# Performance work log

Measured on AMD Instinct MI355X. Metric: run time of the kernel, lower is better.

The kernel has to match this reference:

```python
import jax, jax.numpy as jnp
import numpy as np

B, L, D, DEPTH, FF, VOCAB = 2, 2048, 1024, 4, 4096, 32000

def setup_inputs():
    key = jax.random.key(0)
    ks = jax.random.split(key, 16)
    n = lambda k, s, sc: jax.random.normal(k, s, dtype=jnp.float32) * sc
    sw = 0.01 / float(np.sqrt(D))  # xavier_normal with gain 0.01 on square dims
    return dict(
        tokens=jax.random.randint(ks[0], (B, L), 0, VOCAB),
        emb=n(ks[1], (VOCAB, D), 0.02),
        Wz=n(ks[2], (DEPTH, D, D), sw), bz=jnp.zeros((DEPTH, D)),
        Wza=n(ks[3], (DEPTH, D, D), sw), bza=jnp.zeros((DEPTH, D)),
        Wy=n(ks[4], (DEPTH, D, D), sw), by=jnp.zeros((DEPTH, D)),
        Wya=n(ks[5], (DEPTH, D, D), sw), bya=jnp.zeros((DEPTH, D)),
        lc_re=n(ks[6], (DEPTH, D), 1.0), lc_im=n(ks[7], (DEPTH, D), 1.0),
        g_in=jnp.ones((DEPTH, D)), g_sc=jnp.ones((DEPTH, D)), g_ffn=jnp.ones((DEPTH, D)),
        Wf=n(ks[8], (DEPTH, D, FF), 0.02), bf=jnp.zeros((DEPTH, FF)),
        Wfa=n(ks[9], (DEPTH, D, FF), 0.02), bfa=jnp.zeros((DEPTH, FF)),
        Wfo=n(ks[10], (DEPTH, FF, D), 0.02), bfo=jnp.zeros((DEPTH, D)),
        ln_w=jnp.ones((D,)), ln_b=jnp.zeros((D,)),
        Wout=n(ks[11], (D, VOCAB), 0.02), bout=jnp.zeros((VOCAB,)),
    )

def _silu(x):
    return x * jax.nn.sigmoid(x)

def _rms(x, w, eps=1e-6):
    return x * jax.lax.rsqrt(jnp.mean(x * x, axis=-1, keepdims=True) + eps) * w

def reference(tokens, emb, Wz, bz, Wza, bza, Wy, by, Wya, bya, lc_re, lc_im,
              g_in, g_sc, g_ffn, Wf, bf, Wfa, bfa, Wfo, bfo, ln_w, ln_b, Wout, bout):
    Bq, Lq = tokens.shape
    # Embedding with max_norm=1: torch renorms accessed rows to norm <= 1
    e = emb[tokens]
    nrm = jnp.linalg.norm(e, axis=-1, keepdims=True)
    x = e * jnp.minimum(1.0, 1.0 / jnp.maximum(nrm, 1e-7))
    # Decaying phazor kernel (shared across layers; phazor_angle_scale is a fixed buffer)
    angle = jnp.power(0.001, jnp.linspace(0.0, 1.0, D))
    ln_ph = (1e-5 + 1j * angle).astype(jnp.complex64)      # [D]
    t = jnp.arange(Lq, dtype=jnp.float32)
    ph = jnp.exp(t[:, None] * ln_ph[None, :])              # [L, D] complex
    pf = jnp.fft.fft(ph, n=2 * Lq, axis=0)                 # [2L, D]
    decay = jnp.exp(ln_ph)                                 # [D]
    for i in range(DEPTH):
        # --- SConv sublayer (pre-RMSNorm + residual) ---
        xr = x
        xn = _rms(x, g_sc[i])
        z = (xn @ Wz[i] + bz[i]) * _silu(xn @ Wza[i] + bza[i])
        zf = jnp.fft.fft(z.astype(jnp.complex64), n=2 * Lq, axis=1)
        h = jnp.fft.ifft(zf * pf[None], axis=1)[:, :Lq]    # inner-chunk causal decaying conv
        lc = (lc_re[i] + 1j * lc_im[i]).astype(jnp.complex64)
        h = h + lc[None, None, :] * ph[None] * decay[None, None, :]  # cross-chunk state carry
        y = (_rms(h.real, g_in[i]) @ Wy[i] + by[i]) * _silu(xn @ Wya[i] + bya[i])
        x = xr + y
        # --- FFN SwiGLU sublayer (pre-RMSNorm + residual) ---
        xr = x
        xn = _rms(x, g_ffn[i])
        x = xr + ((xn @ Wf[i] + bf[i]) * _silu(xn @ Wfa[i] + bfa[i])) @ Wfo[i] + bfo[i]
    # Final LayerNorm + vocab projection
    mu = jnp.mean(x, axis=-1, keepdims=True)
    var = jnp.mean((x - mu) ** 2, axis=-1, keepdims=True)
    x = (x - mu) * jax.lax.rsqrt(var + 1e-5) * ln_w + ln_b
    return x @ Wout + bout
```

## Files before the change

### kernel.cpp

```cpp
#include <hip/hip_runtime.h>
#include <math.h>

typedef __attribute__((ext_vector_type(8))) short bf16x8;
typedef __attribute__((ext_vector_type(4))) float f32x4;

#define DEVI __device__ __forceinline__

DEVI short f2bf(float f) {
  unsigned u = __builtin_bit_cast(unsigned, f);
  return (short)((u + 0x7fffu + ((u >> 16) & 1u)) >> 16);
}

DEVI float silu_f(float v) { return v / (1.0f + expf(-v)); }

DEVI void async16(const void* g, void* l) {
  __builtin_amdgcn_global_load_lds(
      (const __attribute__((address_space(1))) void*)g,
      (__attribute__((address_space(3))) void*)l, 16, 0, 0);
}

template <int N>
DEVI void waitvm() { asm volatile("s_waitcnt vmcnt(%0)" ::"i"(N) : "memory"); }
DEVI void barrier_mem() { asm volatile("s_barrier" ::: "memory"); }

template <int NROWT>
DEVI void tile_map(int* bx, int* by) {
  const int nwg = gridDim.x;
  const int lin = blockIdx.x;
  const int q = nwg >> 3;
  const int wgid = (lin & 7) * q + (lin >> 3);
  *by = wgid % NROWT;
  *bx = wgid / NROWT;
}


template <int MODE, int BM, int BN, int NBUF, bool NT>
__global__ __launch_bounds__(256) void gemm_k(const short* __restrict__ A,
                                              const short* __restrict__ BT,
                                              const float* __restrict__ bias,
                                              void* __restrict__ outp,
                                              int N, int K) {
  constexpr int MF = BM / 32, NF = BN / 32;
  constexpr int PBB = (BM + BN) * 64;
  constexpr int DEPTH = NBUF - 1;
  constexpr int L = (BM + BN) / 64;
  __shared__ __align__(16) char lds[NBUF * PBB];
  int bx, by;
  tile_map<4096 / BM>(&bx, &by);
  const int row0 = by * BM, col0 = bx * BN;
  const int t = threadIdx.x, w = t >> 6, lane = t & 63;
  const int wr = w >> 1, wc = w & 1;
  f32x4 acc[MF][NF] = {};

  const int srow = t >> 2;
  const int sslot = (t & 3) ^ ((t >> 3) & 3);
  const char* gA0 = (const char*)A + ((size_t)(row0 + srow) * K) * 2 + sslot * 16;
  const char* gB0 = (const char*)BT + ((size_t)(col0 + srow) * K) * 2 + sslot * 16;
  const size_t ccstep = (size_t)K * 128;
  const int wb = w << 10;
  const int lr = lane & 15, ks = lane >> 4;

  const int NIT = K >> 5;
  auto stage = [&](int buf, int it) {
    char* dst = lds + buf * PBB;
    const size_t io = (size_t)it * 64;
#pragma unroll
    for (int cc = 0; cc < BM / 64; ++cc)
      async16(gA0 + io + cc * ccstep, dst + cc * 4096 + wb);
#pragma unroll
    for (int cc = 0; cc < BN / 64; ++cc)
      async16(gB0 + io + cc * ccstep, dst + BM * 64 + cc * 4096 + wb);
  };

#pragma unroll
  for (int pit = 0; pit < DEPTH; ++pit) stage(pit, pit);

  for (int it = 0; it < NIT; ++it) {
    const int rem = NIT - it;
    if (rem >= DEPTH) waitvm<L * (DEPTH - 1)>();
    else if (rem == 2) waitvm<L>();
    else waitvm<0>();
    barrier_mem();
    if (it + DEPTH < NIT) stage((it + DEPTH) % NBUF, it + DEPTH);
    const char* base = lds + (it % NBUF) * PBB;
    bf16x8 af[MF], bfr[NF];
#pragma unroll
    for (int m = 0; m < MF; ++m) {
      const int r = wr * (BM / 2) + m * 16 + lr;
      af[m] = *(const bf16x8*)(base + r * 64 + ((ks ^ ((r >> 1) & 3)) << 4));
    }
#pragma unroll
    for (int n = 0; n < NF; ++n) {
      const int r = wc * (BN / 2) + n * 16 + lr;
      bfr[n] = *(const bf16x8*)(base + BM * 64 + r * 64 + ((ks ^ ((r >> 1) & 3)) << 4));
    }
#pragma unroll
    for (int m = 0; m < MF; ++m)
#pragma unroll
      for (int n = 0; n < NF; ++n)
        acc[m][n] = __builtin_amdgcn_mfma_f32_16x16x32_bf16(af[m], bfr[n], acc[m][n], 0, 0, 0);
    __builtin_amdgcn_sched_barrier(0);
  }

  const int orow = row0 + wr * (BM / 2) + (ks << 2);
  const int ocol = col0 + wc * (BN / 2) + lr;
#pragma unroll
  for (int m = 0; m < MF; ++m) {
#pragma unroll
    for (int n = 0; n < NF; ++n) {
      const int c = ocol + (n << 4);
      const float bv = bias[c];
#pragma unroll
      for (int i = 0; i < 4; ++i) {
        const int r = orow + (m << 4) + i;
        const size_t idx = (size_t)r * N + c;
        float v = acc[m][n][i] + bv;
        if (MODE == 0) {
          if (NT) __builtin_nontemporal_store(v, &((float*)outp)[idx]);
          else ((float*)outp)[idx] = v;
        } else {
          ((float*)outp)[idx] += v;
        }
      }
    }
  }
}

template <int MODE, int BM, int NBUF>
__global__ __launch_bounds__(256) void gemm2_k(const short* __restrict__ A1,
                                               const short* __restrict__ A2,
                                               const short* __restrict__ BT1,
                                               const short* __restrict__ BT2,
                                               const float* __restrict__ bias1,
                                               const float* __restrict__ bias2,
                                               void* __restrict__ outp,
                                               int N, int K) {
  constexpr bool DUALA = (MODE == 1);
  constexpr int MF = BM / 32;
  constexpr int ABYTES = BM * 64 * (DUALA ? 2 : 1);
  constexpr int PBB = ABYTES + 16384;
  constexpr int DEPTH = NBUF - 1;
  constexpr int L = (DUALA ? 2 * (BM / 64) : (BM / 64)) + 4;
  __shared__ __align__(16) char lds[NBUF * PBB];
  int bx, by;
  tile_map<4096 / BM>(&bx, &by);
  const int row0 = by * BM, col0 = bx << 7;
  const int t = threadIdx.x, w = t >> 6, lane = t & 63;
  const int wr = w >> 1, wc = w & 1;
  f32x4 acc1[MF][4] = {}, acc2[MF][4] = {};

  const int srow = t >> 2;
  const int sslot = (t & 3) ^ ((t >> 3) & 3);
  const size_t arow = ((size_t)(row0 + srow) * K) * 2 + sslot * 16;
  const size_t brow = ((size_t)(col0 + srow) * K) * 2 + sslot * 16;
  const char* gA1 = (const char*)A1 + arow;
  const char* gA2 = (const char*)A2 + arow;
  const char* gB1 = (const char*)BT1 + brow;
  const char* gB2 = (const char*)BT2 + brow;
  const size_t ccstep = (size_t)K * 128;
  const int wb = w << 10;
  const int lr = lane & 15, ks = lane >> 4;

  const int NIT = K >> 5;
  auto stage = [&](int buf, int it) {
    char* dst = lds + buf * PBB;
    const size_t io = (size_t)it * 64;
#pragma unroll
    for (int cc = 0; cc < BM / 64; ++cc) {
      async16(gA1 + io + cc * ccstep, dst + cc * 4096 + wb);
      if constexpr (DUALA)
        async16(gA2 + io + cc * ccstep, dst + BM * 64 + cc * 4096 + wb);
    }
    async16(gB1 + io, dst + ABYTES + wb);
    async16(gB1 + io + ccstep, dst + ABYTES + 4096 + wb);
    async16(gB2 + io, dst + ABYTES + 8192 + wb);
    async16(gB2 + io + ccstep, dst + ABYTES + 8192 + 4096 + wb);
  };

#pragma unroll
  for (int pit = 0; pit < DEPTH; ++pit) stage(pit, pit);

  for (int it = 0; it < NIT; ++it) {
    const int rem = NIT - it;
    if (rem >= DEPTH) waitvm<L * (DEPTH - 1)>();
    else if (rem == 2) waitvm<L>();
    else waitvm<0>();
    barrier_mem();
    if (it + DEPTH < NIT) stage((it + DEPTH) % NBUF, it + DEPTH);
    const char* base = lds + (it % NBUF) * PBB;
    bf16x8 af1[MF], af2[MF], bf1[4], bf2[4];
#pragma unroll
    for (int m = 0; m < MF; ++m) {
      const int r = wr * (BM / 2) + m * 16 + lr;
      const int off = r * 64 + ((ks ^ ((r >> 1) & 3)) << 4);
      af1[m] = *(const bf16x8*)(base + off);
      if constexpr (DUALA) af2[m] = *(const bf16x8*)(base + BM * 64 + off);
    }
#pragma unroll
    for (int n = 0; n < 4; ++n) {
      const int r = wc * 64 + n * 16 + lr;
      const int off = r * 64 + ((ks ^ ((r >> 1) & 3)) << 4);
      bf1[n] = *(const bf16x8*)(base + ABYTES + off);
      bf2[n] = *(const bf16x8*)(base + ABYTES + 8192 + off);
    }
#pragma unroll
    for (int m = 0; m < MF; ++m)
#pragma unroll
      for (int n = 0; n < 4; ++n) {
        acc1[m][n] = __builtin_amdgcn_mfma_f32_16x16x32_bf16(af1[m], bf1[n], acc1[m][n], 0, 0, 0);
        acc2[m][n] = __builtin_amdgcn_mfma_f32_16x16x32_bf16(DUALA ? af2[m] : af1[m], bf2[n],
                                                             acc2[m][n], 0, 0, 0);
      }
    __builtin_amdgcn_sched_barrier(0);
  }

  const int orow = row0 + wr * (BM / 2) + (ks << 2);
  const int ocol = col0 + (wc << 6) + lr;
#pragma unroll
  for (int m = 0; m < MF; ++m) {
#pragma unroll
    for (int n = 0; n < 4; ++n) {
      const int c = ocol + (n << 4);
      const float bv1 = bias1[c], bv2 = bias2[c];
#pragma unroll
      for (int i = 0; i < 4; ++i) {
        const int r = orow + (m << 4) + i;
        const size_t idx = (size_t)r * N + c;
        const float g = (acc1[m][n][i] + bv1) * silu_f(acc2[m][n][i] + bv2);
        if (MODE == 0) ((float*)outp)[idx] = g;
        else if (MODE == 1) ((float*)outp)[idx] += g;
        else ((short*)outp)[idx] = f2bf(g);
      }
    }
  }
}

__global__ __launch_bounds__(256) void transp_k(const float* __restrict__ W,
                                                short* __restrict__ WT,
                                                int R, int C) {
  __shared__ float tile[32][33];
  const size_t moff = (size_t)blockIdx.z * R * C;
  const float* Wp = W + moff;
  short* Tp = WT + moff;
  const int c0 = blockIdx.x << 5, r0 = blockIdx.y << 5;
  const int tx = threadIdx.x, ty = threadIdx.y;
#pragma unroll
  for (int i = 0; i < 4; ++i)
    tile[ty + 8 * i][tx] = Wp[(size_t)(r0 + ty + 8 * i) * C + (c0 + tx)];
  __syncthreads();
#pragma unroll
  for (int i = 0; i < 4; ++i)
    Tp[(size_t)(c0 + ty + 8 * i) * R + (r0 + tx)] = f2bf(tile[tx][ty + 8 * i]);
}

__global__ __launch_bounds__(256) void embed_k(const int* __restrict__ tok,
                                               const float* __restrict__ emb,
                                               float* __restrict__ x) {
  const int row = blockIdx.x, t = threadIdx.x, w = t >> 6, lane = t & 63;
  const int token = tok[row];
  float4 v = ((const float4*)(emb + (size_t)token * 1024))[t];
  float ss = v.x * v.x + v.y * v.y + v.z * v.z + v.w * v.w;
#pragma unroll
  for (int off = 32; off; off >>= 1) ss += __shfl_xor(ss, off, 64);
  __shared__ float red[4];
  if (lane == 0) red[w] = ss;
  __syncthreads();
  const float nrm = sqrtf(red[0] + red[1] + red[2] + red[3]);
  const float sc = fminf(1.0f, 1.0f / fmaxf(nrm, 1e-7f));
  v.x *= sc; v.y *= sc; v.z *= sc; v.w *= sc;
  ((float4*)(x + (size_t)row * 1024))[t] = v;
}

__global__ __launch_bounds__(256) void rms_k(const float* __restrict__ x,
                                             const float* __restrict__ g,
                                             short* __restrict__ o) {
  const int row = blockIdx.x, t = threadIdx.x, w = t >> 6, lane = t & 63;
  float4 v = ((const float4*)(x + (size_t)row * 1024))[t];
  float ss = v.x * v.x + v.y * v.y + v.z * v.z + v.w * v.w;
#pragma unroll
  for (int off = 32; off; off >>= 1) ss += __shfl_xor(ss, off, 64);
  __shared__ float red[4];
  if (lane == 0) red[w] = ss;
  __syncthreads();
  const float sc = rsqrtf((red[0] + red[1] + red[2] + red[3]) * (1.0f / 1024.0f) + 1e-6f);
  float4 gv = ((const float4*)g)[t];
  short4 ov = make_short4(f2bf(v.x * sc * gv.x), f2bf(v.y * sc * gv.y),
                          f2bf(v.z * sc * gv.z), f2bf(v.w * sc * gv.w));
  *(short4*)(o + (size_t)row * 1024 + 4 * t) = ov;
}

__global__ __launch_bounds__(256) void ln_k(const float* __restrict__ x,
                                            const float* __restrict__ lw,
                                            const float* __restrict__ lb,
                                            short* __restrict__ o) {
  const int row = blockIdx.x, t = threadIdx.x, w = t >> 6, lane = t & 63;
  float4 v = ((const float4*)(x + (size_t)row * 1024))[t];
  float s1 = v.x + v.y + v.z + v.w;
  float s2 = v.x * v.x + v.y * v.y + v.z * v.z + v.w * v.w;
#pragma unroll
  for (int off = 32; off; off >>= 1) {
    s1 += __shfl_xor(s1, off, 64);
    s2 += __shfl_xor(s2, off, 64);
  }
  __shared__ float red[8];
  if (lane == 0) { red[w] = s1; red[4 + w] = s2; }
  __syncthreads();
  const float mu = (red[0] + red[1] + red[2] + red[3]) * (1.0f / 1024.0f);
  const float ex2 = (red[4] + red[5] + red[6] + red[7]) * (1.0f / 1024.0f);
  const float rs = rsqrtf(ex2 - mu * mu + 1e-5f);
  float4 wv = ((const float4*)lw)[t];
  float4 bv = ((const float4*)lb)[t];
  short4 ov = make_short4(f2bf((v.x - mu) * rs * wv.x + bv.x),
                          f2bf((v.y - mu) * rs * wv.y + bv.y),
                          f2bf((v.z - mu) * rs * wv.z + bv.z),
                          f2bf((v.w - mu) * rs * wv.w + bv.w));
  *(short4*)(o + (size_t)row * 1024 + 4 * t) = ov;
}

DEVI void decay_of(int d, float* dr, float* di) {
  const float ang = powf(1e-3f, (float)d * (1.0f / 1023.0f));
  float sn, cs;
  sincosf(ang, &sn, &cs);
  const float mag = expf(1e-5f);
  *dr = mag * cs; *di = mag * sn;
}

__global__ __launch_bounds__(256) void s1_k(const float* __restrict__ z,
                                            float* __restrict__ Er, float* __restrict__ Ei) {
  const int d = (blockIdx.x << 8) + threadIdx.x;
  const int c = blockIdx.y, b = blockIdx.z;
  float dr, di;
  decay_of(d, &dr, &di);
  const float* zp = z + ((size_t)(b * 2048 + c * 64) << 10) + d;
  float sr = 0.0f, si = 0.0f;
  for (int k = 0; k < 64; ++k) {
    float zv = zp[(size_t)k << 10];
    float nr = dr * sr - di * si + zv;
    si = dr * si + di * sr;
    sr = nr;
  }
  const int idx = ((b << 5) + c) * 1024 + d;
  Er[idx] = sr; Ei[idx] = si;
}

__global__ __launch_bounds__(256) void s2_k(const float* __restrict__ Er,
                                            const float* __restrict__ Ei,
                                            float* __restrict__ Sr, float* __restrict__ Si) {
  const int gid = (blockIdx.x << 8) + threadIdx.x;
  const int b = gid >> 10, d = gid & 1023;
  float dr, di;
  decay_of(d, &dr, &di);
  float ar = dr, ai = di;
#pragma unroll
  for (int q = 0; q < 6; ++q) { float nr = ar * ar - ai * ai; ai = 2.0f * ar * ai; ar = nr; }
  float sr = 0.0f, si = 0.0f;
  for (int c = 0; c < 32; ++c) {
    const int idx = ((b << 5) + c) * 1024 + d;
    Sr[idx] = sr; Si[idx] = si;
    const float er = Er[idx], ei = Ei[idx];
    const float nr = ar * sr - ai * si + er;
    si = ar * si + ai * sr + ei;
    sr = nr;
  }
}

__global__ __launch_bounds__(256) void s3_k(const float* __restrict__ z,
                                            const float* __restrict__ Sr,
                                            const float* __restrict__ Si,
                                            const float* __restrict__ lcre,
                                            const float* __restrict__ lcim,
                                            float* __restrict__ h) {
  const int d = (blockIdx.x << 8) + threadIdx.x;
  const int c = blockIdx.y, b = blockIdx.z;
  float dr, di;
  decay_of(d, &dr, &di);
  float ar = dr, ai = di;
#pragma unroll
  for (int q = 0; q < 6; ++q) { float nr = ar * ar - ai * ai; ai = 2.0f * ar * ai; ar = nr; }
  float wr = 1.0f, wi = 0.0f, br = ar, bi = ai;
  int e = c;
  while (e) {
    if (e & 1) { float nr = wr * br - wi * bi; wi = wr * bi + wi * br; wr = nr; }
    float nb = br * br - bi * bi; bi = 2.0f * br * bi; br = nb;
    e >>= 1;
  }
  { float nr = wr * dr - wi * di; wi = wr * di + wi * dr; wr = nr; }
  const int idx = ((b << 5) + c) * 1024 + d;
  float sr = Sr[idx], si = Si[idx];
  const float lr_ = lcre[d], li_ = lcim[d];
  const size_t base = ((size_t)(b * 2048 + c * 64) << 10) + d;
  for (int k = 0; k < 64; ++k) {
    const float zv = z[base + ((size_t)k << 10)];
    const float nr = dr * sr - di * si + zv;
    si = dr * si + di * sr;
    sr = nr;
    h[base + ((size_t)k << 10)] = sr + lr_ * wr - li_ * wi;
    const float nw = wr * dr - wi * di;
    wi = wr * di + wi * dr;
    wr = nw;
  }
}

extern "C" void kernel_launch(void* const* d_in, const int* in_sizes, int n_in,
                              void* d_out, int out_size, void* d_ws, size_t ws_size,
                              hipStream_t stream) {
  const int* tokens = (const int*)d_in[0];
  const float* emb = (const float*)d_in[1];
  const float* Wz = (const float*)d_in[2];
  const float* bz = (const float*)d_in[3];
  const float* Wza = (const float*)d_in[4];
  const float* bza = (const float*)d_in[5];
  const float* Wy = (const float*)d_in[6];
  const float* by = (const float*)d_in[7];
  const float* Wya = (const float*)d_in[8];
  const float* bya = (const float*)d_in[9];
  const float* lc_re = (const float*)d_in[10];
  const float* lc_im = (const float*)d_in[11];
  const float* g_in = (const float*)d_in[12];
  const float* g_sc = (const float*)d_in[13];
  const float* g_ffn = (const float*)d_in[14];
  const float* Wf = (const float*)d_in[15];
  const float* bf = (const float*)d_in[16];
  const float* Wfa = (const float*)d_in[17];
  const float* bfa = (const float*)d_in[18];
  const float* Wfo = (const float*)d_in[19];
  const float* bfo = (const float*)d_in[20];
  const float* ln_w = (const float*)d_in[21];
  const float* ln_b = (const float*)d_in[22];
  const float* Wout = (const float*)d_in[23];
  const float* bout = (const float*)d_in[24];

  char* p = (char*)d_ws;
  float* xb = (float*)p;   p += (size_t)4096 * 1024 * 4;
  float* zb = (float*)p;   p += (size_t)4096 * 1024 * 4;
  float* hb = (float*)p;   p += (size_t)4096 * 1024 * 4;
  float* Er = (float*)p;   p += (size_t)2 * 32 * 1024 * 4;
  float* Ei = (float*)p;   p += (size_t)2 * 32 * 1024 * 4;
  float* Sr = (float*)p;   p += (size_t)2 * 32 * 1024 * 4;
  float* Si = (float*)p;   p += (size_t)2 * 32 * 1024 * 4;
  short* xnb = (short*)p;  p += (size_t)4096 * 1024 * 2;
  short* hnb = (short*)p;  p += (size_t)4096 * 1024 * 2;
  short* gb = (short*)p;   p += (size_t)4096 * 4096 * 2;
  short* WzT = (short*)p;  p += (size_t)4 * 1024 * 1024 * 2;
  short* WzaT = (short*)p; p += (size_t)4 * 1024 * 1024 * 2;
  short* WyT = (short*)p;  p += (size_t)4 * 1024 * 1024 * 2;
  short* WyaT = (short*)p; p += (size_t)4 * 1024 * 1024 * 2;
  short* WfT = (short*)p;  p += (size_t)4 * 1024 * 4096 * 2;
  short* WfaT = (short*)p; p += (size_t)4 * 1024 * 4096 * 2;
  short* WfoT = (short*)p; p += (size_t)4 * 1024 * 4096 * 2;
  short* WoutT = (short*)p; p += (size_t)32000 * 1024 * 2;

  const dim3 tb(32, 8);
  transp_k<<<dim3(32, 32, 4), tb, 0, stream>>>(Wz, WzT, 1024, 1024);
  transp_k<<<dim3(32, 32, 4), tb, 0, stream>>>(Wza, WzaT, 1024, 1024);
  transp_k<<<dim3(32, 32, 4), tb, 0, stream>>>(Wy, WyT, 1024, 1024);
  transp_k<<<dim3(32, 32, 4), tb, 0, stream>>>(Wya, WyaT, 1024, 1024);
  transp_k<<<dim3(128, 32, 4), tb, 0, stream>>>(Wf, WfT, 1024, 4096);
  transp_k<<<dim3(128, 32, 4), tb, 0, stream>>>(Wfa, WfaT, 1024, 4096);
  transp_k<<<dim3(32, 128, 4), tb, 0, stream>>>(Wfo, WfoT, 4096, 1024);
  transp_k<<<dim3(1000, 32, 1), tb, 0, stream>>>(Wout, WoutT, 1024, 32000);

  embed_k<<<4096, 256, 0, stream>>>(tokens, emb, xb);

  for (int i = 0; i < 4; ++i) {
    const size_t dd = (size_t)i * 1024 * 1024;
    const size_t dv = (size_t)i * 1024;
    const size_t dw = (size_t)i * 1024 * 4096;
    const size_t df = (size_t)i * 4096;
    rms_k<<<4096, 256, 0, stream>>>(xb, g_sc + dv, xnb);
    gemm2_k<0, 64, 3><<<512, 256, 0, stream>>>(xnb, xnb, WzT + dd, WzaT + dd, bz + dv, bza + dv,
                                               zb, 1024, 1024);
    s1_k<<<dim3(4, 32, 2), 256, 0, stream>>>(zb, Er, Ei);
    s2_k<<<8, 256, 0, stream>>>(Er, Ei, Sr, Si);
    s3_k<<<dim3(4, 32, 2), 256, 0, stream>>>(zb, Sr, Si, lc_re + dv, lc_im + dv, hb);
    rms_k<<<4096, 256, 0, stream>>>(hb, g_in + dv, hnb);
    gemm2_k<1, 64, 2><<<512, 256, 0, stream>>>(hnb, xnb, WyT + dd, WyaT + dd, by + dv, bya + dv,
                                               xb, 1024, 1024);
    rms_k<<<4096, 256, 0, stream>>>(xb, g_ffn + dv, xnb);
    gemm2_k<2, 64, 3><<<2048, 256, 0, stream>>>(xnb, xnb, WfT + dw, WfaT + dw, bf + df, bfa + df,
                                                gb, 4096, 1024);
    gemm_k<4, 64, 128, 4, false><<<512, 256, 0, stream>>>(gb, WfoT + dw, bfo + dv, xb, 1024, 4096);
  }

  ln_k<<<4096, 256, 0, stream>>>(xb, ln_w, ln_b, xnb);
  gemm_k<0, 128, 128, 4, true><<<8000, 256, 0, stream>>>(xnb, WoutT, bout, (float*)d_out,
                                                         32000, 1024);

  (void)in_sizes; (void)n_in; (void)out_size; (void)ws_size;
}
```

Baseline: 1.869 ms.

## Generalize GEMM warp tiling, enlarge tiles, and store scan intermediates in bf16

The GEMM kernels now take per-wave tile dimensions as template parameters and use larger block tiles (128x128, and 128x256 for the vocab projection), with launch bounds set for two blocks per CU. This raises data reuse per block and cuts how often operands are reloaded from global memory. The z and h intermediates of the phazor scan are now stored in bf16 instead of fp32, halving their memory traffic, and rms_k gains a bf16 input path to read them. In exchange there are fewer blocks per launch (256 for some GEMMs), which can leave CUs idle, more register pressure, and some precision loss in the scan inputs. The pipeline wait counts were also adjusted for the three-buffer depth.

```diff
diff --git a/kernel.cpp b/kernel.cpp
--- a/kernel.cpp
+++ b/kernel.cpp
@@ -9,6 +9,10 @@
 DEVI short f2bf(float f) {
   unsigned u = __builtin_bit_cast(unsigned, f);
   return (short)((u + 0x7fffu + ((u >> 16) & 1u)) >> 16);
+}
+DEVI float bf2f(short s) {
+  unsigned u = ((unsigned)(unsigned short)s) << 16;
+  return __builtin_bit_cast(float, u);
 }
 
 DEVI float silu_f(float v) { return v / (1.0f + expf(-v)); }
@@ -34,22 +38,24 @@
 }
 
 
-template <int MODE, int BM, int BN, int NBUF, bool NT>
-__global__ __launch_bounds__(256) void gemm_k(const short* __restrict__ A,
-                                              const short* __restrict__ BT,
-                                              const float* __restrict__ bias,
-                                              void* __restrict__ outp,
-                                              int N, int K) {
-  constexpr int MF = BM / 32, NF = BN / 32;
+template <int MODE, int BM, int BN, int WM, int WN, int NBUF, bool NT>
+__global__ __launch_bounds__(256, 2) void gemm_k(const short* __restrict__ A,
+                                                 const short* __restrict__ BT,
+                                                 const float* __restrict__ bias,
+                                                 void* __restrict__ outp,
+                                                 int N, int K) {
+  constexpr int MF = WM / 16, NF = WN / 16;
+  constexpr int NWN = BN / WN;
   constexpr int PBB = (BM + BN) * 64;
   constexpr int DEPTH = NBUF - 1;
   constexpr int L = (BM + BN) / 64;
+  static_assert((BM / WM) * (BN / WN) == 4, "4 waves");
   __shared__ __align__(16) char lds[NBUF * PBB];
   int bx, by;
   tile_map<4096 / BM>(&bx, &by);
   const int row0 = by * BM, col0 = bx * BN;
   const int t = threadIdx.x, w = t >> 6, lane = t & 63;
-  const int wr = w >> 1, wc = w & 1;
+  const int wr = w / NWN, wc = w % NWN;
   f32x4 acc[MF][NF] = {};
 
   const int srow = t >> 2;
@@ -77,8 +83,8 @@
 
   for (int it = 0; it < NIT; ++it) {
     const int rem = NIT - it;
-    if (rem >= DEPTH) waitvm<L * (DEPTH - 1)>();
-    else if (rem == 2) waitvm<L>();
+    if (rem >= DEPTH + 1) waitvm<L * (DEPTH - 1)>();
+    else if (rem >= 2) waitvm<L>();
     else waitvm<0>();
     barrier_mem();
     if (it + DEPTH < NIT) stage((it + DEPTH) % NBUF, it + DEPTH);
@@ -86,12 +92,12 @@
     bf16x8 af[MF], bfr[NF];
 #pragma unroll
     for (int m = 0; m < MF; ++m) {
-      const int r = wr * (BM / 2) + m * 16 + lr;
+      const int r = wr * WM + m * 16 + lr;
       af[m] = *(const bf16x8*)(base + r * 64 + ((ks ^ ((r >> 1) & 3)) << 4));
     }
 #pragma unroll
     for (int n = 0; n < NF; ++n) {
-      const int r = wc * (BN / 2) + n * 16 + lr;
+      const int r = wc * WN + n * 16 + lr;
       bfr[n] = *(const bf16x8*)(base + BM * 64 + r * 64 + ((ks ^ ((r >> 1) & 3)) << 4));
     }
 #pragma unroll
@@ -102,8 +108,8 @@
     __builtin_amdgcn_sched_barrier(0);
   }
 
-  const int orow = row0 + wr * (BM / 2) + (ks << 2);
-  const int ocol = col0 + wc * (BN / 2) + lr;
+  const int orow = row0 + wr * WM + (ks << 2);
+  const int ocol = col0 + wc * WN + lr;
 #pragma unroll
   for (int m = 0; m < MF; ++m) {
 #pragma unroll
@@ -126,28 +132,30 @@
   }
 }
 
-template <int MODE, int BM, int NBUF>
-__global__ __launch_bounds__(256) void gemm2_k(const short* __restrict__ A1,
-                                               const short* __restrict__ A2,
-                                               const short* __restrict__ BT1,
-                                               const short* __restrict__ BT2,
-                                               const float* __restrict__ bias1,
-                                               const float* __restrict__ bias2,
-                                               void* __restrict__ outp,
-                                               int N, int K) {
+template <int MODE, int BM, int BN, int WM, int WN, int NBUF>
+__global__ __launch_bounds__(256, 2) void gemm2_k(const short* __restrict__ A1,
+                                                  const short* __restrict__ A2,
+                                                  const short* __restrict__ BT1,
+                                                  const short* __restrict__ BT2,
+                                                  const float* __restrict__ bias1,
+                                                  const float* __restrict__ bias2,
+                                                  void* __restrict__ outp,
+                                                  int N, int K) {
   constexpr bool DUALA = (MODE == 1);
-  constexpr int MF = BM / 32;
+  constexpr int MF = WM / 16, NF = WN / 16;
+  constexpr int NWN = BN / WN;
   constexpr int ABYTES = BM * 64 * (DUALA ? 2 : 1);
-  constexpr int PBB = ABYTES + 16384;
+  constexpr int PBB = ABYTES + 2 * BN * 64;
   constexpr int DEPTH = NBUF - 1;
-  constexpr int L = (DUALA ? 2 * (BM / 64) : (BM / 64)) + 4;
+  constexpr int L = ((DUALA ? 2 : 1) * BM + 2 * BN) / 64;
+  static_assert((BM / WM) * (BN / WN) == 4, "4 waves");
   __shared__ __align__(16) char lds[NBUF * PBB];
   int bx, by;
   tile_map<4096 / BM>(&bx, &by);
-  const int row0 = by * BM, col0 = bx << 7;
+  const int row0 = by * BM, col0 = bx * BN;
   const int t = threadIdx.x, w = t >> 6, lane = t & 63;
-  const int wr = w >> 1, wc = w & 1;
-  f32x4 acc1[MF][4] = {}, acc2[MF][4] = {};
+  const int wr = w / NWN, wc = w % NWN;
+  f32x4 acc1[MF][NF] = {}, acc2[MF][NF] = {};
 
   const int srow = t >> 2;
   const int sslot = (t & 3) ^ ((t >> 3) & 3);
@@ -171,10 +179,11 @@
       if constexpr (DUALA)
         async16(gA2 + io + cc * ccstep, dst + BM * 64 + cc * 4096 + wb);
     }
-    async16(gB1 + io, dst + ABYTES + wb);
-    async16(gB1 + io + ccstep, dst + ABYTES + 4096 + wb);
-    async16(gB2 + io, dst + ABYTES + 8192 + wb);
-    async16(gB2 + io + ccstep, dst + ABYTES + 8192 + 4096 + wb);
+#pragma unroll
+    for (int cc = 0; cc < BN / 64; ++cc) {
+      async16(gB1 + io + cc * ccstep, dst + ABYTES + cc * 4096 + wb);
+      async16(gB2 + io + cc * ccstep, dst + ABYTES + BN * 64 + cc * 4096 + wb);
+    }
   };
 
 #pragma unroll
@@ -182,31 +191,31 @@
 
   for (int it = 0; it < NIT; ++it) {
     const int rem = NIT - it;
-    if (rem >= DEPTH) waitvm<L * (DEPTH - 1)>();
-    else if (rem == 2) waitvm<L>();
+    if (rem >= DEPTH + 1) waitvm<L * (DEPTH - 1)>();
+    else if (rem >= 2) waitvm<L>();
     else waitvm<0>();
     barrier_mem();
     if (it + DEPTH < NIT) stage((it + DEPTH) % NBUF, it + DEPTH);
     const char* base = lds + (it % NBUF) * PBB;
-    bf16x8 af1[MF], af2[MF], bf1[4], bf2[4];
+    bf16x8 af1[MF], af2[MF], bf1[NF], bf2[NF];
 #pragma unroll
     for (int m = 0; m < MF; ++m) {
-      const int r = wr * (BM / 2) + m * 16 + lr;
+      const int r = wr * WM + m * 16 + lr;
       const int off = r * 64 + ((ks ^ ((r >> 1) & 3)) << 4);
       af1[m] = *(const bf16x8*)(base + off);
       if constexpr (DUALA) af2[m] = *(const bf16x8*)(base + BM * 64 + off);
     }
 #pragma unroll
-    for (int n = 0; n < 4; ++n) {
-      const int r = wc * 64 + n * 16 + lr;
+    for (int n = 0; n < NF; ++n) {
+      const int r = wc * WN + n * 16 + lr;
       const int off = r * 64 + ((ks ^ ((r >> 1) & 3)) << 4);
       bf1[n] = *(const bf16x8*)(base + ABYTES + off);
-      bf2[n] = *(const bf16x8*)(base + ABYTES + 8192 + off);
+      bf2[n] = *(const bf16x8*)(base + ABYTES + BN * 64 + off);
     }
 #pragma unroll
     for (int m = 0; m < MF; ++m)
 #pragma unroll
-      for (int n = 0; n < 4; ++n) {
+      for (int n = 0; n < NF; ++n) {
         acc1[m][n] = __builtin_amdgcn_mfma_f32_16x16x32_bf16(af1[m], bf1[n], acc1[m][n], 0, 0, 0);
         acc2[m][n] = __builtin_amdgcn_mfma_f32_16x16x32_bf16(DUALA ? af2[m] : af1[m], bf2[n],
                                                              acc2[m][n], 0, 0, 0);
@@ -214,12 +223,12 @@
     __builtin_amdgcn_sched_barrier(0);
   }
 
-  const int orow = row0 + wr * (BM / 2) + (ks << 2);
-  const int ocol = col0 + (wc << 6) + lr;
+  const int orow = row0 + wr * WM + (ks << 2);
+  const int ocol = col0 + wc * WN + lr;
 #pragma unroll
   for (int m = 0; m < MF; ++m) {
 #pragma unroll
-    for (int n = 0; n < 4; ++n) {
+    for (int n = 0; n < NF; ++n) {
       const int c = ocol + (n << 4);
       const float bv1 = bias1[c], bv2 = bias2[c];
 #pragma unroll
@@ -227,8 +236,7 @@
         const int r = orow + (m << 4) + i;
         const size_t idx = (size_t)r * N + c;
         const float g = (acc1[m][n][i] + bv1) * silu_f(acc2[m][n][i] + bv2);
-        if (MODE == 0) ((float*)outp)[idx] = g;
-        else if (MODE == 1) ((float*)outp)[idx] += g;
+        if (MODE == 1) ((float*)outp)[idx] += g;
         else ((short*)outp)[idx] = f2bf(g);
       }
     }
@@ -271,12 +279,20 @@
   ((float4*)(x + (size_t)row * 1024))[t] = v;
 }
 
-__global__ __launch_bounds__(256) void rms_k(const float* __restrict__ x,
+template <int BF>
+__global__ __launch_bounds__(256) void rms_k(const void* __restrict__ xin,
                                              const float* __restrict__ g,
                                              short* __restrict__ o) {
   const int row = blockIdx.x, t = threadIdx.x, w = t >> 6, lane = t & 63;
-  float4 v = ((const float4*)(x + (size_t)row * 1024))[t];
-  float ss = v.x * v.x + v.y * v.y + v.z * v.z + v.w * v.w;
+  float v0, v1, v2, v3;
+  if (BF) {
+    short4 s = ((const short4*)((const short*)xin + (size_t)row * 1024))[t];
+    v0 = bf2f(s.x); v1 = bf2f(s.y); v2 = bf2f(s.z); v3 = bf2f(s.w);
+  } else {
+    float4 v = ((const float4*)((const float*)xin + (size_t)row * 1024))[t];
+    v0 = v.x; v1 = v.y; v2 = v.z; v3 = v.w;
+  }
+  float ss = v0 * v0 + v1 * v1 + v2 * v2 + v3 * v3;
 #pragma unroll
   for (int off = 32; off; off >>= 1) ss += __shfl_xor(ss, off, 64);
   __shared__ float red[4];
@@ -284,8 +300,8 @@
   __syncthreads();
   const float sc = rsqrtf((red[0] + red[1] + red[2] + red[3]) * (1.0f / 1024.0f) + 1e-6f);
   float4 gv = ((const float4*)g)[t];
-  short4 ov = make_short4(f2bf(v.x * sc * gv.x), f2bf(v.y * sc * gv.y),
-                          f2bf(v.z * sc * gv.z), f2bf(v.w * sc * gv.w));
+  short4 ov = make_short4(f2bf(v0 * sc * gv.x), f2bf(v1 * sc * gv.y),
+                          f2bf(v2 * sc * gv.z), f2bf(v3 * sc * gv.w));
   *(short4*)(o + (size_t)row * 1024 + 4 * t) = ov;
 }
 
@@ -325,16 +341,16 @@
   *dr = mag * cs; *di = mag * sn;
 }
 
-__global__ __launch_bounds__(256) void s1_k(const float* __restrict__ z,
+__global__ __launch_bounds__(256) void s1_k(const short* __restrict__ z,
                                             float* __restrict__ Er, float* __restrict__ Ei) {
   const int d = (blockIdx.x << 8) + threadIdx.x;
   const int c = blockIdx.y, b = blockIdx.z;
   float dr, di;
   decay_of(d, &dr, &di);
-  const float* zp = z + ((size_t)(b * 2048 + c * 64) << 10) + d;
+  const short* zp = z + ((size_t)(b * 2048 + c * 64) << 10) + d;
   float sr = 0.0f, si = 0.0f;
   for (int k = 0; k < 64; ++k) {
-    float zv = zp[(size_t)k << 10];
+    float zv = bf2f(zp[(size_t)k << 10]);
     float nr = dr * sr - di * si + zv;
     si = dr * si + di * sr;
     sr = nr;
@@ -364,12 +380,12 @@
   }
 }
 
-__global__ __launch_bounds__(256) void s3_k(const float* __restrict__ z,
+__global__ __launch_bounds__(256) void s3_k(const short* __restrict__ z,
                                             const float* __restrict__ Sr,
                                             const float* __restrict__ Si,
                                             const float* __restrict__ lcre,
                                             const float* __restrict__ lcim,
-                                            float* __restrict__ h) {
+                                            short* __restrict__ h) {
   const int d = (blockIdx.x << 8) + threadIdx.x;
   const int c = blockIdx.y, b = blockIdx.z;
   float dr, di;
@@ -390,11 +406,11 @@
   const float lr_ = lcre[d], li_ = lcim[d];
   const size_t base = ((size_t)(b * 2048 + c * 64) << 10) + d;
   for (int k = 0; k < 64; ++k) {
-    const float zv = z[base + ((size_t)k << 10)];
+    const float zv = bf2f(z[base + ((size_t)k << 10)]);
     const float nr = dr * sr - di * si + zv;
     si = dr * si + di * sr;
     sr = nr;
-    h[base + ((size_t)k << 10)] = sr + lr_ * wr - li_ * wi;
+    h[base + ((size_t)k << 10)] = f2bf(sr + lr_ * wr - li_ * wi);
     const float nw = wr * dr - wi * di;
     wi = wr * di + wi * dr;
     wr = nw;
@@ -432,8 +448,8 @@
 
   char* p = (char*)d_ws;
   float* xb = (float*)p;   p += (size_t)4096 * 1024 * 4;
-  float* zb = (float*)p;   p += (size_t)4096 * 1024 * 4;
-  float* hb = (float*)p;   p += (size_t)4096 * 1024 * 4;
+  short* zb = (short*)p;   p += (size_t)4096 * 1024 * 2;
+  short* hb = (short*)p;   p += (size_t)4096 * 1024 * 2;
   float* Er = (float*)p;   p += (size_t)2 * 32 * 1024 * 4;
   float* Ei = (float*)p;   p += (size_t)2 * 32 * 1024 * 4;
   float* Sr = (float*)p;   p += (size_t)2 * 32 * 1024 * 4;
@@ -467,24 +483,25 @@
     const size_t dv = (size_t)i * 1024;
     const size_t dw = (size_t)i * 1024 * 4096;
     const size_t df = (size_t)i * 4096;
-    rms_k<<<4096, 256, 0, stream>>>(xb, g_sc + dv, xnb);
-    gemm2_k<0, 64, 3><<<512, 256, 0, stream>>>(xnb, xnb, WzT + dd, WzaT + dd, bz + dv, bza + dv,
-                                               zb, 1024, 1024);
+    rms_k<0><<<4096, 256, 0, stream>>>(xb, g_sc + dv, xnb);
+    gemm2_k<2, 128, 128, 64, 64, 3><<<256, 256, 0, stream>>>(
+        xnb, xnb, WzT + dd, WzaT + dd, bz + dv, bza + dv, zb, 1024, 1024);
     s1_k<<<dim3(4, 32, 2), 256, 0, stream>>>(zb, Er, Ei);
     s2_k<<<8, 256, 0, stream>>>(Er, Ei, Sr, Si);
     s3_k<<<dim3(4, 32, 2), 256, 0, stream>>>(zb, Sr, Si, lc_re + dv, lc_im + dv, hb);
-    rms_k<<<4096, 256, 0, stream>>>(hb, g_in + dv, hnb);
-    gemm2_k<1, 64, 2><<<512, 256, 0, stream>>>(hnb, xnb, WyT + dd, WyaT + dd, by + dv, bya + dv,
-                                               xb, 1024, 1024);
-    rms_k<<<4096, 256, 0, stream>>>(xb, g_ffn + dv, xnb);
-    gemm2_k<2, 64, 3><<<2048, 256, 0, stream>>>(xnb, xnb, WfT + dw, WfaT + dw, bf + df, bfa + df,
-                                                gb, 4096, 1024);
-    gemm_k<4, 64, 128, 4, false><<<512, 256, 0, stream>>>(gb, WfoT + dw, bfo + dv, xb, 1024, 4096);
+    rms_k<1><<<4096, 256, 0, stream>>>(hb, g_in + dv, hnb);
+    gemm2_k<1, 64, 128, 32, 64, 3><<<512, 256, 0, stream>>>(
+        hnb, xnb, WyT + dd, WyaT + dd, by + dv, bya + dv, xb, 1024, 1024);
+    rms_k<0><<<4096, 256, 0, stream>>>(xb, g_ffn + dv, xnb);
+    gemm2_k<2, 128, 128, 64, 64, 3><<<1024, 256, 0, stream>>>(
+        xnb, xnb, WfT + dw, WfaT + dw, bf + df, bfa + df, gb, 4096, 1024);
+    gemm_k<4, 128, 128, 64, 64, 3, false><<<256, 256, 0, stream>>>(
+        gb, WfoT + dw, bfo + dv, xb, 1024, 4096);
   }
 
   ln_k<<<4096, 256, 0, stream>>>(xb, ln_w, ln_b, xnb);
-  gemm_k<0, 128, 128, 4, true><<<8000, 256, 0, stream>>>(xnb, WoutT, bout, (float*)d_out,
-                                                         32000, 1024);
+  gemm_k<0, 128, 256, 128, 64, 3, true><<<4000, 256, 0, stream>>>(
+      xnb, WoutT, bout, (float*)d_out, 32000, 1024);
 
   (void)in_sizes; (void)n_in; (void)out_size; (void)ws_size;
 }
```

Result: faster. 1.642 ms (-12.1%).
